# Kernel tuning notes

Measured on AMD Instinct MI355X. Metric: run time of the kernel, lower is better.

Reference implementation:

```python
import jax, jax.numpy as jnp
import numpy as np
import math

B, S, D, H = 8, 1024, 512, 8  # batch, seqlen, d_model, heads
DK = D // H

def setup_inputs() -> dict:
    key = jax.random.key(0)
    ks = jax.random.split(key, 8)
    std = 1.0 / math.sqrt(D)
    return {
        "x": jax.random.normal(ks[0], (B, S, D), jnp.float32),
        "utT_similarities": jax.random.uniform(ks[1], (B, S, S), jnp.float32),
        "Wk": jax.random.normal(ks[2], (D, D), jnp.float32) * std,
        "bk": jnp.zeros((D,), jnp.float32),
        "Wv": jax.random.normal(ks[3], (D, D), jnp.float32) * std,
        "bv": jnp.zeros((D,), jnp.float32),
        "Wo": jax.random.normal(ks[4], (D, D), jnp.float32) * std,
        "bo": jnp.zeros((D,), jnp.float32),
        "gammas": jax.random.normal(ks[5], (H, 1, 1), jnp.float32) * 0.1,
    }

def reference(x, utT_similarities, Wk, bk, Wv, bv, Wo, bo, gammas):
    b, s, d = x.shape
    h = gammas.shape[0]
    dk = d // h
    NEG = -1e32

    def split_heads(t):  # [b,s,d] -> [b,h,s,dk]
        return t.reshape(b, s, h, dk).transpose(0, 2, 1, 3)

    # kq_same=True: q and k share k_linear
    q = split_heads(x @ Wk.T + bk)
    k = q
    v = split_heads(x @ Wv.T + bv)

    scores = jnp.einsum('bhid,bhjd->bhij', q, k) / jnp.sqrt(jnp.float32(dk))
    scores = scores * utT_similarities[:, None, :, :]

    mask = jnp.tril(jnp.ones((s, s), dtype=bool))  # causal, incl diagonal (mask=1)

    # distance-decay block (no_grad in torch -> stop_gradient)
    s_ = jax.nn.softmax(jnp.where(mask, scores, NEG), axis=-1) * mask
    distcum = jnp.cumsum(s_, axis=-1)
    disttotal = jnp.sum(s_, axis=-1, keepdims=True)
    idx = jnp.arange(s)
    position_effect = jnp.abs(idx[None, :] - idx[:, None]).astype(jnp.float32)  # [s,s]
    dist_scores = jnp.sqrt(jnp.clip((disttotal - distcum) * position_effect, 0.0, None))
    dist_scores = jax.lax.stop_gradient(dist_scores)

    gamma = -jax.nn.softplus(gammas)[None]  # [1,h,1,1]
    total_effect = jnp.clip(jnp.exp(dist_scores * gamma), 1e-5, 1e5)

    scores = jax.nn.softmax(jnp.where(mask, scores * total_effect, NEG), axis=-1)
    # zero_pad=False (mask=1 path), dropout is identity in eval
    out = jnp.einsum('bhij,bhjd->bhid', scores, v)
    out = out.transpose(0, 2, 1, 3).reshape(b, s, d)
    return out @ Wo.T + bo
```

## Files before the change

### kernel.cpp

```cpp
#include <hip/hip_runtime.h>
#include <math.h>

#define NB   8
#define SS   1024
#define DD   512
#define HH   8
#define DKK  64
#define NEGF (-3.0e38f)

#define QSTR 88
#define SSTR 257
#define PSTR 280
#define WSTR 40

typedef _Float16 half8 __attribute__((ext_vector_type(8)));
typedef float    f32x4 __attribute__((ext_vector_type(4)));

__global__ __launch_bounds__(256) void gemm_qv(
    const float* __restrict__ x,
    const float* __restrict__ Wk, const float* __restrict__ bk,
    const float* __restrict__ Wv, const float* __restrict__ bv,
    _Float16* __restrict__ q_ws, _Float16* __restrict__ vt_ws)
{
    __shared__ __align__(16) _Float16 Asm[64 * WSTR];
    __shared__ __align__(16) _Float16 Bsm[64 * WSTR];

    const int m0  = blockIdx.x * 64;
    const int n0c = blockIdx.y * 64;
    const bool is_v = (n0c >= DD);
    const float* __restrict__ Wp = is_v ? Wv : Wk;
    const float* __restrict__ bp = is_v ? bv : bk;
    const int n0 = n0c & (DD - 1);

    const int tid  = threadIdx.x;
    const int w    = tid >> 6;
    const int lane = tid & 63;
    const int quad = lane >> 4;
    const int n    = lane & 15;
    const int wm   = w >> 1, wn = w & 1;

    const int srow = tid >> 2;
    const int sc8  = (tid & 3) * 8;

    f32x4 acc[2][2] = {{{0.f,0.f,0.f,0.f},{0.f,0.f,0.f,0.f}},
                       {{0.f,0.f,0.f,0.f},{0.f,0.f,0.f,0.f}}};

    for (int k0 = 0; k0 < DD; k0 += 32) {
        __syncthreads();
        {
            const float* src = &x[(size_t)(m0 + srow) * DD + k0 + sc8];
            float4 f0 = *(const float4*)&src[0];
            float4 f1 = *(const float4*)&src[4];
            half8 hv = {(_Float16)f0.x,(_Float16)f0.y,(_Float16)f0.z,(_Float16)f0.w,
                        (_Float16)f1.x,(_Float16)f1.y,(_Float16)f1.z,(_Float16)f1.w};
            *(half8*)&Asm[srow * WSTR + sc8] = hv;
        }
        {
            const float* src = &Wp[(size_t)(n0 + srow) * DD + k0 + sc8];
            float4 f0 = *(const float4*)&src[0];
            float4 f1 = *(const float4*)&src[4];
            half8 hv = {(_Float16)f0.x,(_Float16)f0.y,(_Float16)f0.z,(_Float16)f0.w,
                        (_Float16)f1.x,(_Float16)f1.y,(_Float16)f1.z,(_Float16)f1.w};
            *(half8*)&Bsm[srow * WSTR + sc8] = hv;
        }
        __syncthreads();
        half8 a0 = *(const half8*)&Asm[(wm*32 +  0 + n) * WSTR + quad*8];
        half8 a1 = *(const half8*)&Asm[(wm*32 + 16 + n) * WSTR + quad*8];
        half8 b0 = *(const half8*)&Bsm[(wn*32 +  0 + n) * WSTR + quad*8];
        half8 b1 = *(const half8*)&Bsm[(wn*32 + 16 + n) * WSTR + quad*8];
        acc[0][0] = __builtin_amdgcn_mfma_f32_16x16x32_f16(a0, b0, acc[0][0], 0,0,0);
        acc[0][1] = __builtin_amdgcn_mfma_f32_16x16x32_f16(a0, b1, acc[0][1], 0,0,0);
        acc[1][0] = __builtin_amdgcn_mfma_f32_16x16x32_f16(a1, b0, acc[1][0], 0,0,0);
        acc[1][1] = __builtin_amdgcn_mfma_f32_16x16x32_f16(a1, b1, acc[1][1], 0,0,0);
    }

    const int h = n0 >> 6;
    #pragma unroll
    for (int tm = 0; tm < 2; ++tm) {
        #pragma unroll
        for (int tn = 0; tn < 2; ++tn) {
            const int dk = wn*32 + tn*16 + n;
            const float bias = bp[n0 + dk];
            const int gbase = m0 + wm*32 + tm*16 + quad*4;
            const int bidx  = gbase >> 10;
            const int sr    = gbase & (SS - 1);
            if (!is_v) {
                #pragma unroll
                for (int reg = 0; reg < 4; ++reg)
                    q_ws[((size_t)(bidx * HH + h) * SS + sr + reg) * DKK + dk] =
                        (_Float16)(acc[tm][tn][reg] + bias);
            } else {
                _Float16 h4[4];
                #pragma unroll
                for (int reg = 0; reg < 4; ++reg)
                    h4[reg] = (_Float16)(acc[tm][tn][reg] + bias);
                *(uint2*)&vt_ws[((size_t)(bidx * HH + h) * DKK + dk) * SS + sr] =
                    *(uint2*)h4;
            }
        }
    }
}

__global__ __launch_bounds__(256) void gemm_out(
    const float* __restrict__ A,
    const float* __restrict__ Wo, const float* __restrict__ bo,
    float* __restrict__ out)
{
    __shared__ __align__(16) _Float16 Asm[64 * WSTR];
    __shared__ __align__(16) _Float16 Bsm[64 * WSTR];

    const int m0 = blockIdx.x * 64;
    const int n0 = blockIdx.y * 64;

    const int tid  = threadIdx.x;
    const int w    = tid >> 6;
    const int lane = tid & 63;
    const int quad = lane >> 4;
    const int n    = lane & 15;
    const int wm   = w >> 1, wn = w & 1;

    const int srow = tid >> 2;
    const int sc8  = (tid & 3) * 8;

    f32x4 acc[2][2] = {{{0.f,0.f,0.f,0.f},{0.f,0.f,0.f,0.f}},
                       {{0.f,0.f,0.f,0.f},{0.f,0.f,0.f,0.f}}};

    for (int k0 = 0; k0 < DD; k0 += 32) {
        __syncthreads();
        {
            const float* src = &A[(size_t)(m0 + srow) * DD + k0 + sc8];
            float4 f0 = *(const float4*)&src[0];
            float4 f1 = *(const float4*)&src[4];
            half8 hv = {(_Float16)f0.x,(_Float16)f0.y,(_Float16)f0.z,(_Float16)f0.w,
                        (_Float16)f1.x,(_Float16)f1.y,(_Float16)f1.z,(_Float16)f1.w};
            *(half8*)&Asm[srow * WSTR + sc8] = hv;
        }
        {
            const float* src = &Wo[(size_t)(n0 + srow) * DD + k0 + sc8];
            float4 f0 = *(const float4*)&src[0];
            float4 f1 = *(const float4*)&src[4];
            half8 hv = {(_Float16)f0.x,(_Float16)f0.y,(_Float16)f0.z,(_Float16)f0.w,
                        (_Float16)f1.x,(_Float16)f1.y,(_Float16)f1.z,(_Float16)f1.w};
            *(half8*)&Bsm[srow * WSTR + sc8] = hv;
        }
        __syncthreads();
        half8 a0 = *(const half8*)&Asm[(wm*32 +  0 + n) * WSTR + quad*8];
        half8 a1 = *(const half8*)&Asm[(wm*32 + 16 + n) * WSTR + quad*8];
        half8 b0 = *(const half8*)&Bsm[(wn*32 +  0 + n) * WSTR + quad*8];
        half8 b1 = *(const half8*)&Bsm[(wn*32 + 16 + n) * WSTR + quad*8];
        acc[0][0] = __builtin_amdgcn_mfma_f32_16x16x32_f16(a0, b0, acc[0][0], 0,0,0);
        acc[0][1] = __builtin_amdgcn_mfma_f32_16x16x32_f16(a0, b1, acc[0][1], 0,0,0);
        acc[1][0] = __builtin_amdgcn_mfma_f32_16x16x32_f16(a1, b0, acc[1][0], 0,0,0);
        acc[1][1] = __builtin_amdgcn_mfma_f32_16x16x32_f16(a1, b1, acc[1][1], 0,0,0);
    }

    #pragma unroll
    for (int tm = 0; tm < 2; ++tm) {
        #pragma unroll
        for (int tn = 0; tn < 2; ++tn) {
            const int col  = n0 + wn*32 + tn*16 + n;
            const float bias = bo[col];
            #pragma unroll
            for (int reg = 0; reg < 4; ++reg) {
                const int grow = m0 + wm*32 + tm*16 + quad*4 + reg;
                out[(size_t)grow * DD + col] = acc[tm][tn][reg] + bias;
            }
        }
    }
}

__global__ __launch_bounds__(1024) void attn_mfma(
    const _Float16* __restrict__ q,
    const _Float16* __restrict__ vt,
    const float* __restrict__ utT,
    const float* __restrict__ gammas,
    float* __restrict__ attn)
{
    __shared__ __align__(16) float    s_lds[2 * 16 * SSTR];
    __shared__ __align__(16) _Float16 q_lds[16 * QSTR];
    _Float16* p_lds = (_Float16*)s_lds;

    const int tid  = threadIdx.x;
    const int w    = tid >> 6;
    const int lane = tid & 63;
    const int quad = lane >> 4;
    const int n    = lane & 15;
    const int bh   = blockIdx.y;
    const int b    = bh >> 3;
    const int h    = bh & 7;
    const int r0   = blockIdx.x * 16;

    const _Float16* __restrict__ kq  = q  + (size_t)bh * SS * DKK;
    const _Float16* __restrict__ vtp = vt + (size_t)bh * DKK * SS;

    const int nchunk = (r0 + 16 + 255) >> 8;
    const int nt     = nchunk * 4;

    if (tid < 256) {
        const int row = tid >> 4;
        const int c   = tid & 15;
        *(uint2*)&q_lds[row * QSTR + c * 4] =
            *(const uint2*)&kq[(size_t)(r0 + row) * DKK + c * 4];
    }
    __syncthreads();

    float sreg[16];
    #pragma unroll
    for (int t2 = 0; t2 < 16; ++t2) sreg[t2] = NEGF;

    #pragma unroll
    for (int c0 = 0; c0 < 4; ++c0) {
        if (c0 < nchunk) {
            const int j0  = c0 * 256;
            const int buf = (c0 & 1) * 16 * SSTR;
            const int jbase = j0 + w * 16;
            if (jbase <= r0 + 15) {
                const _Float16* krow = &kq[(size_t)(jbase + n) * DKK];
                half8 b0 = *(const half8*)&krow[quad * 8];
                half8 b1 = *(const half8*)&krow[32 + quad * 8];
                half8 a0 = *(const half8*)&q_lds[n * QSTR + quad * 8];
                half8 a1 = *(const half8*)&q_lds[n * QSTR + 32 + quad * 8];
                f32x4 d = {0.f, 0.f, 0.f, 0.f};
                d = __builtin_amdgcn_mfma_f32_16x16x32_f16(a0, b0, d, 0, 0, 0);
                d = __builtin_amdgcn_mfma_f32_16x16x32_f16(a1, b1, d, 0, 0, 0);
                const int j = jbase + n;
                #pragma unroll
                for (int reg = 0; reg < 4; ++reg) {
                    const int i = r0 + quad * 4 + reg;
                    float val = NEGF;
                    if (j <= i)
                        val = d[reg] * 0.125f * utT[((size_t)b * SS + i) * SS + j];
                    s_lds[buf + (quad * 4 + reg) * SSTR + w * 16 + n] = val;
                }
            } else {
                #pragma unroll
                for (int reg = 0; reg < 4; ++reg)
                    s_lds[buf + (quad * 4 + reg) * SSTR + w * 16 + n] = NEGF;
            }
            __syncthreads();
            #pragma unroll
            for (int ttl = 0; ttl < 4; ++ttl)
                sreg[c0 * 4 + ttl] = s_lds[buf + w * SSTR + ttl * 64 + lane];
        }
    }

    const int i_row = r0 + w;

    float m1 = NEGF;
    #pragma unroll
    for (int t2 = 0; t2 < 16; ++t2) if (t2 < nt) m1 = fmaxf(m1, sreg[t2]);
    #pragma unroll
    for (int o = 32; o >= 1; o >>= 1) m1 = fmaxf(m1, __shfl_xor(m1, o));

    float ee[16];
    float z1 = 0.f;
    #pragma unroll
    for (int t2 = 0; t2 < 16; ++t2) {
        float e = 0.f;
        if (t2 < nt) {
            const int j = t2 * 64 + lane;
            if (j <= i_row) e = __expf(sreg[t2] - m1);
        }
        ee[t2] = e;
        z1 += e;
    }
    #pragma unroll
    for (int o = 32; o >= 1; o >>= 1) z1 += __shfl_xor(z1, o);
    const float inv_z1 = 1.0f / z1;

    const float g     = gammas[h];
    const float gamma = -log1pf(__expf(g));

    float carry = 0.f;
    float m2 = NEGF;
    #pragma unroll
    for (int t2 = 0; t2 < 16; ++t2) {
        if (t2 < nt) {
            float xv = ee[t2];
            #pragma unroll
            for (int o = 1; o < 64; o <<= 1) {
                float y = __shfl_up(xv, (unsigned)o);
                if (lane >= o) xv += y;
            }
            const float tile_tot = __shfl(xv, 63);
            const float csum = (carry + xv) * inv_z1;
            carry += tile_tot;

            const int j = t2 * 64 + lane;
            const float pe = (float)(i_row - j);
            const float dd = fmaxf((1.0f - csum) * pe, 0.0f);
            float te = __expf(sqrtf(dd) * gamma);
            te = fminf(fmaxf(te, 1e-5f), 1e5f);
            const float nsv = (j <= i_row) ? sreg[t2] * te : NEGF;
            ee[t2] = nsv;
            m2 = fmaxf(m2, nsv);
        }
    }
    #pragma unroll
    for (int o = 32; o >= 1; o >>= 1) m2 = fmaxf(m2, __shfl_xor(m2, o));

    float z2 = 0.f;
    #pragma unroll
    for (int t2 = 0; t2 < 16; ++t2) {
        if (t2 < nt) {
            ee[t2] = __expf(ee[t2] - m2);
            z2 += ee[t2];
        }
    }
    #pragma unroll
    for (int o = 32; o >= 1; o >>= 1) z2 += __shfl_xor(z2, o);
    const float inv_z2 = 1.0f / z2;
    #pragma unroll
    for (int t2 = 0; t2 < 16; ++t2) if (t2 < nt) ee[t2] *= inv_z2;

    __syncthreads();

    f32x4 oacc = {0.f, 0.f, 0.f, 0.f};
    #pragma unroll
    for (int c0 = 0; c0 < 4; ++c0) {
        if (c0 < nchunk) {
            const int j0 = c0 * 256;
            const int pb = (c0 & 1) * 16 * PSTR;
            #pragma unroll
            for (int ttl = 0; ttl < 4; ++ttl)
                p_lds[pb + w * PSTR + ttl * 64 + lane] = (_Float16)ee[c0 * 4 + ttl];
            __syncthreads();
            if (w < 4) {
                int nkt = (r0 + 16 - j0 + 31) >> 5;
                nkt = (nkt > 8) ? 8 : nkt;
                const _Float16* vrow = &vtp[(size_t)(w * 16 + n) * SS + j0];
                for (int kt = 0; kt < nkt; ++kt) {
                    half8 a  = *(const half8*)&p_lds[pb + n * PSTR + kt * 32 + quad * 8];
                    half8 bb = *(const half8*)&vrow[kt * 32 + quad * 8];
                    oacc = __builtin_amdgcn_mfma_f32_16x16x32_f16(a, bb, oacc, 0, 0, 0);
                }
            }
        }
    }

    if (w < 4) {
        #pragma unroll
        for (int reg = 0; reg < 4; ++reg) {
            const int i = r0 + quad * 4 + reg;
            attn[(((size_t)b * SS + i) * HH + h) * DKK + w * 16 + n] = oacc[reg];
        }
    }
}

extern "C" void kernel_launch(void* const* d_in, const int* in_sizes, int n_in,
                              void* d_out, int out_size, void* d_ws, size_t ws_size,
                              hipStream_t stream) {
    const float* x      = (const float*)d_in[0];
    const float* utT    = (const float*)d_in[1];
    const float* Wk     = (const float*)d_in[2];
    const float* bk     = (const float*)d_in[3];
    const float* Wv     = (const float*)d_in[4];
    const float* bv     = (const float*)d_in[5];
    const float* Wo     = (const float*)d_in[6];
    const float* bo     = (const float*)d_in[7];
    const float* gammas = (const float*)d_in[8];
    float* out = (float*)d_out;

    const size_t per = (size_t)NB * HH * SS * DKK;
    _Float16* q_ws   = (_Float16*)d_ws;
    _Float16* vt_ws  = q_ws + per;
    float*    attn_ws = (float*)(vt_ws + per);

    dim3 g1(128, 16);
    gemm_qv<<<g1, dim3(256), 0, stream>>>(x, Wk, bk, Wv, bv, q_ws, vt_ws);

    dim3 g2(SS / 16, NB * HH);
    attn_mfma<<<g2, dim3(1024), 0, stream>>>(q_ws, vt_ws, utT, gammas, attn_ws);

    dim3 g3(128, 8);
    gemm_out<<<g3, dim3(256), 0, stream>>>(attn_ws, Wo, bo, out);
}
```

Measured before the change: 338.8 us.

## Split PV MFMA across all waves with LDS reduction, coalesce utT loads

Result: slower. 445.9 us (+31.6%).

```diff
diff --git a/kernel.cpp b/kernel.cpp
--- a/kernel.cpp
+++ b/kernel.cpp
@@ -178,6 +178,7 @@
 {
     __shared__ __align__(16) float    s_lds[2 * 16 * SSTR];
     __shared__ __align__(16) _Float16 q_lds[16 * QSTR];
+    __shared__ __align__(16) f32x4    o_red[16 * 64];
     _Float16* p_lds = (_Float16*)s_lds;
 
     const int tid  = threadIdx.x;
@@ -194,7 +195,10 @@
     const _Float16* __restrict__ vtp = vt + (size_t)bh * DKK * SS;
 
     const int nchunk = (r0 + 16 + 255) >> 8;
-    const int nt     = nchunk * 4;
+
+    const int i_row = r0 + w;
+    const int tmax  = i_row >> 6;
+    const float* __restrict__ ut_row = utT + ((size_t)b * SS + i_row) * SS;
 
     if (tid < 256) {
         const int row = tid >> 4;
@@ -203,6 +207,9 @@
             *(const uint2*)&kq[(size_t)(r0 + row) * DKK + c * 4];
     }
     __syncthreads();
+
+    const half8 a0 = *(const half8*)&q_lds[n * QSTR + quad * 8];
+    const half8 a1 = *(const half8*)&q_lds[n * QSTR + 32 + quad * 8];
 
     float sreg[16];
     #pragma unroll
@@ -218,51 +225,45 @@
                 const _Float16* krow = &kq[(size_t)(jbase + n) * DKK];
                 half8 b0 = *(const half8*)&krow[quad * 8];
                 half8 b1 = *(const half8*)&krow[32 + quad * 8];
-                half8 a0 = *(const half8*)&q_lds[n * QSTR + quad * 8];
-                half8 a1 = *(const half8*)&q_lds[n * QSTR + 32 + quad * 8];
                 f32x4 d = {0.f, 0.f, 0.f, 0.f};
                 d = __builtin_amdgcn_mfma_f32_16x16x32_f16(a0, b0, d, 0, 0, 0);
                 d = __builtin_amdgcn_mfma_f32_16x16x32_f16(a1, b1, d, 0, 0, 0);
-                const int j = jbase + n;
-                #pragma unroll
-                for (int reg = 0; reg < 4; ++reg) {
-                    const int i = r0 + quad * 4 + reg;
-                    float val = NEGF;
-                    if (j <= i)
-                        val = d[reg] * 0.125f * utT[((size_t)b * SS + i) * SS + j];
-                    s_lds[buf + (quad * 4 + reg) * SSTR + w * 16 + n] = val;
-                }
-            } else {
                 #pragma unroll
                 for (int reg = 0; reg < 4; ++reg)
-                    s_lds[buf + (quad * 4 + reg) * SSTR + w * 16 + n] = NEGF;
+                    s_lds[buf + (quad * 4 + reg) * SSTR + w * 16 + n] = d[reg] * 0.125f;
             }
             __syncthreads();
             #pragma unroll
-            for (int ttl = 0; ttl < 4; ++ttl)
-                sreg[c0 * 4 + ttl] = s_lds[buf + w * SSTR + ttl * 64 + lane];
-        }
-    }
-
-    const int i_row = r0 + w;
+            for (int ttl = 0; ttl < 4; ++ttl) {
+                const int tt = c0 * 4 + ttl;
+                if (tt <= tmax) {
+                    const int j = tt * 64 + lane;
+                    const float raw = s_lds[buf + w * SSTR + ttl * 64 + lane];
+                    const float ut  = ut_row[j];
+                    sreg[tt] = (j <= i_row) ? raw * ut : NEGF;
+                }
+            }
+        }
+    }
 
     float m1 = NEGF;
     #pragma unroll
-    for (int t2 = 0; t2 < 16; ++t2) if (t2 < nt) m1 = fmaxf(m1, sreg[t2]);
+    for (int t2 = 0; t2 < 16; ++t2) if (t2 <= tmax) m1 = fmaxf(m1, sreg[t2]);
     #pragma unroll
     for (int o = 32; o >= 1; o >>= 1) m1 = fmaxf(m1, __shfl_xor(m1, o));
 
     float ee[16];
+    #pragma unroll
+    for (int t2 = 0; t2 < 16; ++t2) ee[t2] = 0.f;
     float z1 = 0.f;
     #pragma unroll
     for (int t2 = 0; t2 < 16; ++t2) {
-        float e = 0.f;
-        if (t2 < nt) {
+        if (t2 <= tmax) {
             const int j = t2 * 64 + lane;
-            if (j <= i_row) e = __expf(sreg[t2] - m1);
-        }
-        ee[t2] = e;
-        z1 += e;
+            const float e = (j <= i_row) ? __expf(sreg[t2] - m1) : 0.f;
+            ee[t2] = e;
+            z1 += e;
+        }
     }
     #pragma unroll
     for (int o = 32; o >= 1; o >>= 1) z1 += __shfl_xor(z1, o);
@@ -275,7 +276,7 @@
     float m2 = NEGF;
     #pragma unroll
     for (int t2 = 0; t2 < 16; ++t2) {
-        if (t2 < nt) {
+        if (t2 <= tmax) {
             float xv = ee[t2];
             #pragma unroll
             for (int o = 1; o < 64; o <<= 1) {
@@ -302,7 +303,7 @@
     float z2 = 0.f;
     #pragma unroll
     for (int t2 = 0; t2 < 16; ++t2) {
-        if (t2 < nt) {
+        if (t2 <= tmax) {
             ee[t2] = __expf(ee[t2] - m2);
             z2 += ee[t2];
         }
@@ -311,10 +312,12 @@
     for (int o = 32; o >= 1; o >>= 1) z2 += __shfl_xor(z2, o);
     const float inv_z2 = 1.0f / z2;
     #pragma unroll
-    for (int t2 = 0; t2 < 16; ++t2) if (t2 < nt) ee[t2] *= inv_z2;
+    for (int t2 = 0; t2 < 16; ++t2) if (t2 <= tmax) ee[t2] *= inv_z2;
 
     __syncthreads();
 
+    const int dslice = w & 3;
+    const int kgroup = w >> 2;
     f32x4 oacc = {0.f, 0.f, 0.f, 0.f};
     #pragma unroll
     for (int c0 = 0; c0 < 4; ++c0) {
@@ -325,11 +328,13 @@
             for (int ttl = 0; ttl < 4; ++ttl)
                 p_lds[pb + w * PSTR + ttl * 64 + lane] = (_Float16)ee[c0 * 4 + ttl];
             __syncthreads();
-            if (w < 4) {
-                int nkt = (r0 + 16 - j0 + 31) >> 5;
-                nkt = (nkt > 8) ? 8 : nkt;
-                const _Float16* vrow = &vtp[(size_t)(w * 16 + n) * SS + j0];
-                for (int kt = 0; kt < nkt; ++kt) {
+            int nkt = (r0 + 16 - j0 + 31) >> 5;
+            nkt = (nkt > 8) ? 8 : nkt;
+            const _Float16* vrow = &vtp[(size_t)(dslice * 16 + n) * SS + j0];
+            #pragma unroll
+            for (int kk = 0; kk < 2; ++kk) {
+                const int kt = kgroup + kk * 4;
+                if (kt < nkt) {
                     half8 a  = *(const half8*)&p_lds[pb + n * PSTR + kt * 32 + quad * 8];
                     half8 bb = *(const half8*)&vrow[kt * 32 + quad * 8];
                     oacc = __builtin_amdgcn_mfma_f32_16x16x32_f16(a, bb, oacc, 0, 0, 0);
@@ -338,11 +343,19 @@
         }
     }
 
+    o_red[w * 64 + lane] = oacc;
+    __syncthreads();
+
     if (w < 4) {
+        f32x4 r0v = o_red[(w     ) * 64 + lane];
+        f32x4 r1v = o_red[(w +  4) * 64 + lane];
+        f32x4 r2v = o_red[(w +  8) * 64 + lane];
+        f32x4 r3v = o_red[(w + 12) * 64 + lane];
+        f32x4 tot = (r0v + r1v) + (r2v + r3v);
         #pragma unroll
         for (int reg = 0; reg < 4; ++reg) {
             const int i = r0 + quad * 4 + reg;
-            attn[(((size_t)b * SS + i) * HH + h) * DKK + w * 16 + n] = oacc[reg];
+            attn[(((size_t)b * SS + i) * HH + h) * DKK + w * 16 + n] = tot[reg];
         }
     }
 }
```
